# Kernel tuning notes

Hardware: AMD Instinct MI355X
Metric: run time of the kernel (lower is better)

Reference implementation:

```python
import jax, jax.numpy as jnp
import numpy as np

B, N, C = 2, 2048, 256
H_DIM, W_DIM = 64, 176


def _lin_init(k, fan_in, shape):
    return jax.random.normal(k, shape, dtype=jnp.float32) * (1.0 / np.sqrt(fan_in))


def setup_inputs() -> dict:
    key = jax.random.key(0)
    ks = jax.random.split(key, 12)
    # gaussian_data: (B, N, 14); positions [:3], sigma_x at 5, sigma_y at 6, weight at 12
    z = jax.random.uniform(ks[0], (B, N), minval=1.0, maxval=40.0)
    x = jax.random.uniform(ks[1], (B, N), minval=-0.6, maxval=0.6) * z
    y = jax.random.uniform(ks[2], (B, N), minval=-0.4, maxval=0.4) * z
    g = jax.random.normal(ks[3], (B, N, 14), dtype=jnp.float32)
    g = g.at[..., 0].set(x).at[..., 1].set(y).at[..., 2].set(z)
    g = g.at[..., 5].set(jax.random.uniform(ks[4], (B, N), minval=5.0, maxval=50.0))
    g = g.at[..., 6].set(jax.random.uniform(ks[5], (B, N), minval=5.0, maxval=50.0))
    g = g.at[..., 12].set(jax.random.uniform(ks[6], (B, N), minval=0.5, maxval=1.5))
    # pinhole intrinsic: fx=fy=1000, cx=880, cy=320
    intrinsic = jnp.array([[1000.0, 0.0, 880.0], [0.0, 1000.0, 320.0], [0.0, 0.0, 1.0]], dtype=jnp.float32)
    pk = jax.random.split(ks[7], 5)
    return {
        "gaussian_data": g,
        "intrinsic": intrinsic,
        "enc_w1": _lin_init(pk[0], 14, (14, 64)), "enc_b1": jnp.zeros((64,), jnp.float32),
        "enc_w2": _lin_init(pk[1], 64, (64, 128)), "enc_b2": jnp.zeros((128,), jnp.float32),
        "enc_w3": _lin_init(pk[2], 128, (128, C)), "enc_b3": jnp.zeros((C,), jnp.float32),
        "ft_w1": _lin_init(pk[3], C, (C, C)), "ft_b1": jnp.zeros((C,), jnp.float32),
        "ft_w2": _lin_init(pk[4], C, (C, C)), "ft_b2": jnp.zeros((C,), jnp.float32),
        "H": H_DIM, "W": W_DIM,
    }


def reference(gaussian_data, intrinsic, enc_w1, enc_b1, enc_w2, enc_b2, enc_w3, enc_b3,
              ft_w1, ft_b1, ft_w2, ft_b2, H, W):
    # Encoder MLP (dropout = identity in eval): (B,N,14) -> (B,N,C)
    h = jax.nn.relu(gaussian_data @ enc_w1 + enc_b1)
    h = jax.nn.relu(h @ enc_w2 + enc_b2)
    feats = h @ enc_w3 + enc_b3
    # feature_transform inside GaussianRadarProjection
    feats_t = jax.nn.relu(feats @ ft_w1 + ft_b1) @ ft_w2 + ft_b2  # (B,N,C)

    pos = gaussian_data[..., :3]                      # (B,N,3)
    valid = pos[..., 2] > 0.1                         # (B,N)
    proj = jnp.einsum('ij,bnj->bni', intrinsic, pos)  # (B,N,3)
    pts2d = proj[..., :2] / (proj[..., 2:3] + 1e-6)   # (B,N,2)
    scale_x = W / intrinsic[0, 2] / 2
    scale_y = H / intrinsic[1, 2] / 2
    px = pts2d[..., 0] * scale_x                      # (B,N)
    py = pts2d[..., 1] * scale_y
    inb = (px >= 0) & (px < W) & (py >= 0) & (py < H)
    mask = valid & inb                                # (B,N)

    sx = jnp.maximum(gaussian_data[..., 5] * scale_x, 1.0)  # (B,N)
    sy = jnp.maximum(gaussian_data[..., 6] * scale_y, 1.0)
    w = gaussian_data[..., 12]                               # (B,N)

    xg = jnp.arange(W, dtype=jnp.float32)
    yg = jnp.arange(H, dtype=jnp.float32)
    dx2 = ((xg[None, None, :] - px[..., None]) / sx[..., None]) ** 2  # (B,N,W)
    dy2 = ((yg[None, None, :] - py[..., None]) / sy[..., None]) ** 2  # (B,N,H)
    dist = dy2[..., :, None] + dx2[..., None, :]                      # (B,N,H,W)
    gw = jnp.exp(-0.5 * dist) * w[..., None, None]
    gw = gw * (dist < 9.0).astype(gw.dtype) * mask[..., None, None].astype(gw.dtype)

    density = jnp.sum(gw, axis=1)[:, None]                             # (B,1,H,W)
    feature_map = jnp.einsum('bnc,bnhw->bchw', feats_t, gw)            # (B,C,H,W)
    avg_sigma = (sx + sy) / 2                                          # (B,N)
    uncertainty = jnp.sum(gw * avg_sigma[..., None, None], axis=1)[:, None]

    density = jnp.clip(density, 1e-6)
    return feature_map / density, uncertainty / density, density
```

## Files before the change

### kernel.cpp

```cpp
#include <hip/hip_runtime.h>
#include <cstdint>
#include <cstddef>

#define B_ 2
#define N_ 2048
#define C_ 256
#define H_ 64
#define W_ 176
#define TW 16
#define NTX 11
#define NYB 32
#define NTILES2 (B_*NYB*NTX)
#define CAP 1024
#define SA 260
#define FS 40
#define CSTRIDE 16

typedef unsigned short ushort_t;
typedef short bf16x8 __attribute__((ext_vector_type(8)));
typedef float f32x4  __attribute__((ext_vector_type(4)));

__device__ __forceinline__ short f2bf(float f)
{
    unsigned u = __float_as_uint(f);
    return (short)((u + 0x7FFFu + ((u >> 16) & 1u)) >> 16);
}

__global__ __launch_bounds__(256)
void prep_kernel(const float* __restrict__ w3f, const float* __restrict__ fw1f,
                 const float* __restrict__ fw2f,
                 short* __restrict__ wt3, short* __restrict__ wt4,
                 short* __restrict__ wt5, int* __restrict__ counts)
{
    const int gid = blockIdx.x * 256 + threadIdx.x;
    if (gid < NTILES2 * CSTRIDE) counts[gid] = 0;
    for (int e = gid; e < 163840; e += 65536) {
        if (e < 32768) {
            const int k = e >> 8, n = e & 255;
            wt3[n * 128 + k] = f2bf(w3f[e]);
        } else if (e < 98304) {
            const int e2 = e - 32768;
            const int k = e2 >> 8, n = e2 & 255;
            wt4[n * 256 + k] = f2bf(fw1f[e2]);
        } else {
            const int e2 = e - 98304;
            const int k = e2 >> 8, n = e2 & 255;
            wt5[n * 256 + k] = f2bf(fw2f[e2]);
        }
    }
}

template<int K>
__device__ __forceinline__ void mfma_acc(const short* __restrict__ wt,
                                         const float* actIn, f32x4 (&acc)[2],
                                         int wv_, int quad, int ln15)
{
    bf16x8 wreg[K / 16];
#pragma unroll
    for (int ks = 0; ks < K / 32; ++ks) {
        const int kb = ks * 32 + quad * 8;
#pragma unroll
        for (int tt = 0; tt < 2; ++tt) {
            const int n0 = (wv_ * 2 + tt) * 16;
            wreg[ks * 2 + tt] = *(const bf16x8*)&wt[(size_t)(n0 + ln15) * K + kb];
        }
    }
#pragma unroll
    for (int ks = 0; ks < K / 32; ++ks) {
        const int kb = ks * 32 + quad * 8;
        const float4 a0 = *(const float4*)&actIn[ln15 * SA + kb];
        const float4 a1 = *(const float4*)&actIn[ln15 * SA + kb + 4];
        bf16x8 af = { f2bf(a0.x), f2bf(a0.y), f2bf(a0.z), f2bf(a0.w),
                      f2bf(a1.x), f2bf(a1.y), f2bf(a1.z), f2bf(a1.w) };
#pragma unroll
        for (int tt = 0; tt < 2; ++tt)
            acc[tt] = __builtin_amdgcn_mfma_f32_16x16x32_bf16(af, wreg[ks * 2 + tt],
                                                              acc[tt], 0, 0, 0);
    }
}

__global__ __launch_bounds__(512, 4)
void pb_mlp_kernel(const float* __restrict__ g, const float* __restrict__ intr,
                   const float* __restrict__ w1, const float* __restrict__ b1,
                   const float* __restrict__ w2, const float* __restrict__ b2,
                   const short* __restrict__ wt3, const float* __restrict__ b3,
                   const short* __restrict__ wt4, const float* __restrict__ fb1,
                   const short* __restrict__ wt5, const float* __restrict__ fb2,
                   ushort_t* __restrict__ ftb,
                   float* __restrict__ pp, int* __restrict__ counts,
                   ushort_t* __restrict__ lists)
{
    __shared__ __align__(16) float A_[16 * SA];
    __shared__ __align__(16) float Bb[16 * SA];
    const int tid = threadIdx.x;

    if (blockIdx.x < 256) {
        const int row0 = blockIdx.x * 16;
        const int lane = tid & 63;
        const int wv_  = tid >> 6;
        const int quad = lane >> 4;
        const int ln15 = lane & 15;

        if (tid < 224) {
            const int k = tid / 16, m = tid % 16;
            A_[m * SA + k] = g[(size_t)(row0 + m) * 14 + k];
        }
        __syncthreads();

        {
            const int col = tid & 63;
            const int m0  = (tid >> 6) * 2;
            float acc[2];
            const float bv = b1[col];
            acc[0] = bv; acc[1] = bv;
#pragma unroll
            for (int k = 0; k < 14; ++k) {
                const float wv = w1[k * 64 + col];
                acc[0] = fmaf(A_[(m0 + 0) * SA + k], wv, acc[0]);
                acc[1] = fmaf(A_[(m0 + 1) * SA + k], wv, acc[1]);
            }
            Bb[(m0 + 0) * SA + col] = fmaxf(acc[0], 0.f);
            Bb[(m0 + 1) * SA + col] = fmaxf(acc[1], 0.f);
        }
        __syncthreads();

        {
            const int col = tid & 127;
            const int m0  = (tid >> 7) * 4;
            float acc[4];
            const float bv = b2[col];
#pragma unroll
            for (int r = 0; r < 4; ++r) acc[r] = bv;
#pragma unroll 4
            for (int kq = 0; kq < 16; ++kq) {
                float wv[4];
#pragma unroll
                for (int jj = 0; jj < 4; ++jj) wv[jj] = w2[(4 * kq + jj) * 128 + col];
#pragma unroll
                for (int r = 0; r < 4; ++r) {
                    const float4 a4 = *(const float4*)&Bb[(m0 + r) * SA + 4 * kq];
                    acc[r] = fmaf(a4.x, wv[0], acc[r]);
                    acc[r] = fmaf(a4.y, wv[1], acc[r]);
                    acc[r] = fmaf(a4.z, wv[2], acc[r]);
                    acc[r] = fmaf(a4.w, wv[3], acc[r]);
                }
            }
#pragma unroll
            for (int r = 0; r < 4; ++r)
                A_[(m0 + r) * SA + col] = fmaxf(acc[r], 0.f);
        }
        __syncthreads();

        {
            f32x4 acc[2] = {{0,0,0,0},{0,0,0,0}};
            mfma_acc<128>(wt3, A_, acc, wv_, quad, ln15);
            __syncthreads();
#pragma unroll
            for (int tt = 0; tt < 2; ++tt) {
                const int n = (wv_ * 2 + tt) * 16 + ln15;
                const float bv = b3[n];
#pragma unroll
                for (int r = 0; r < 4; ++r)
                    Bb[(quad * 4 + r) * SA + n] = acc[tt][r] + bv;
            }
        }
        __syncthreads();

        {
            f32x4 acc[2] = {{0,0,0,0},{0,0,0,0}};
            mfma_acc<256>(wt4, Bb, acc, wv_, quad, ln15);
            __syncthreads();
#pragma unroll
            for (int tt = 0; tt < 2; ++tt) {
                const int n = (wv_ * 2 + tt) * 16 + ln15;
                const float bv = fb1[n];
#pragma unroll
                for (int r = 0; r < 4; ++r)
                    A_[(quad * 4 + r) * SA + n] = fmaxf(acc[tt][r] + bv, 0.f);
            }
        }
        __syncthreads();

        {
            f32x4 acc[2] = {{0,0,0,0},{0,0,0,0}};
            mfma_acc<256>(wt5, A_, acc, wv_, quad, ln15);
#pragma unroll
            for (int tt = 0; tt < 2; ++tt) {
                const int n = (wv_ * 2 + tt) * 16 + ln15;
                const float bv = fb2[n];
#pragma unroll
                for (int r = 0; r < 4; ++r)
                    ftb[(size_t)(row0 + quad * 4 + r) * 256 + n] =
                        (ushort_t)f2bf(acc[tt][r] + bv);
            }
        }
        return;
    }

    const int i = (blockIdx.x - 256) * 16 + (tid >> 5);
    const int j = tid & 31;
    const float* gi = g + (size_t)i * 14;
    const float x = gi[0], y = gi[1], z = gi[2];
    const float s5 = gi[5], s6 = gi[6], wv = gi[12];
    const float k00 = intr[0], k01 = intr[1], k02 = intr[2];
    const float k10 = intr[3], k11 = intr[4], k12 = intr[5];
    const float k20 = intr[6], k21 = intr[7], k22 = intr[8];
    const float projx = k00 * x + k01 * y + k02 * z;
    const float projy = k10 * x + k11 * y + k12 * z;
    const float projz = k20 * x + k21 * y + k22 * z;
    const float inv = 1.f / (projz + 1e-6f);
    const float scale_x = (float)W_ / k02 * 0.5f;
    const float scale_y = (float)H_ / k12 * 0.5f;
    const float px = projx * inv * scale_x;
    const float py = projy * inv * scale_y;
    const bool valid = z > 0.1f;
    const bool inb = (px >= 0.f) && (px < (float)W_) && (py >= 0.f) && (py < (float)H_);
    const bool mask = valid && inb;
    const float sx = fmaxf(s5 * scale_x, 1.f);
    const float sy = fmaxf(s6 * scale_y, 1.f);
    if (j == 0) {
        float4* o = (float4*)(pp + (size_t)i * 8);
        o[0] = make_float4(px, py, 1.f / sx, 1.f / sy);
        o[1] = make_float4(wv, 0.5f * (sx + sy), 0.f, 0.f);
    }
    if (!mask) return;
    const float rx = 3.f * sx, ry = 3.f * sy;
    const int ymin = max(0, (int)floorf(py - ry));
    const int ymax = min(H_ - 1, (int)ceilf(py + ry));
    const int bmin = ymin >> 1, bmax = ymax >> 1;
    const int band = bmin + j;
    if (band > bmax) return;
    const int tmin = max(0, (int)floorf((px - rx - (float)(TW - 1)) * (1.f / TW)));
    const int tmax = min(NTX - 1, (int)ceilf((px + rx) * (1.f / TW)));
    const int b = i / N_, n = i - b * N_;
    for (int t = tmin; t <= tmax; ++t) {
        const int tile = (b * NYB + band) * NTX + t;
        const int slot = atomicAdd(&counts[tile * CSTRIDE], 1);
        if (slot < CAP) lists[(size_t)tile * CAP + slot] = (ushort_t)n;
    }
}

__global__ __launch_bounds__(256)
void splat_kernel(const float* __restrict__ pp, const ushort_t* __restrict__ lists,
                  const int* __restrict__ counts, const ushort_t* __restrict__ ftb,
                  float* __restrict__ out)
{
    __shared__ __align__(16) ushort_t feats_t[2][256 * FS];
    __shared__ __align__(16) ushort_t gw_t[2][32 * FS];

    const int tid = threadIdx.x;
    const int qb = blockIdx.x;
    const int b  = qb & 1;
    const int t_ = qb >> 1;
    const int yr = t_ / NTX, xr = t_ % NTX;
    const int yh = (yr + 1) >> 1;
    const int yb = (yr & 1) ? (16 - yh) : (16 + yh);
    const int xh = (xr + 1) >> 1;
    const int txi = (xr & 1) ? (5 - xh) : (5 + xh);
    const int bid = (b * NYB + yb) * NTX + txi;
    const int y0 = yb * 2, x0 = txi * TW;

    const int cnt = min(counts[bid * CSTRIDE], CAP);
    const ushort_t* mylist = lists + (size_t)bid * CAP;
    const int gs   = tid >> 5;
    const int px32 = tid & 31;
    const float fy = (float)(y0 + (px32 >> 4));
    const float fx = (float)(x0 + (px32 & 15));
    const int chg = tid >> 4;
    const int qp  = tid & 15;
    const int bN = b * N_;
    const int lane = tid & 63;
    const int wv_  = tid >> 6;
    const int quad = lane >> 4;
    const int ln15 = lane & 15;

    f32x4 acc[2][4];
#pragma unroll
    for (int mt = 0; mt < 2; ++mt)
#pragma unroll
        for (int nt = 0; nt < 4; ++nt) acc[mt][nt] = (f32x4){0.f, 0.f, 0.f, 0.f};
    float densp = 0.f, uncp = 0.f;

    uint4 ra0, ra1, rb0, rb1;
    const int nchunks = (cnt + 31) >> 5;

    if (cnt > 0) {
        const float4* pv = (const float4*)pp;
        {
            const int n0 = mylist[min(2 * qp, cnt - 1)];
            const int n1 = mylist[min(2 * qp + 1, cnt - 1)];
            const uint4* f0 = (const uint4*)(ftb + ((size_t)(bN + n0) << 8) + chg * 16);
            const uint4* f1 = (const uint4*)(ftb + ((size_t)(bN + n1) << 8) + chg * 16);
            ra0 = f0[0]; ra1 = f0[1];
            rb0 = f1[0]; rb1 = f1[1];
        }
        for (int c = 0; c < nchunks; ++c) {
            const int buf = c & 1;
#pragma unroll
            for (int jj = 0; jj < 4; ++jj) {
                const int q = 8 * jj + gs;
                const int qi = c * 32 + q;
                const int n = mylist[min(qi, cnt - 1)];
                const float4 e0 = pv[(size_t)(bN + n) * 2 + 0];
                const float4 e1 = pv[(size_t)(bN + n) * 2 + 1];
                const float dyn = (fy - e0.y) * e0.w;
                const float dxn = (fx - e0.x) * e0.z;
                const float dist = dyn * dyn + dxn * dxn;
                float gv = 0.f;
                if (dist < 9.f) gv = __expf(-0.5f * dist) * e1.x;
                if (qi >= cnt) gv = 0.f;
                gw_t[buf][px32 * FS + q] = (ushort_t)f2bf(gv);
                densp += gv;
                uncp  += gv * e1.y;
            }
            {
                uint* dst = (uint*)&feats_t[buf][0];
#pragma unroll
                for (int jj = 0; jj < 4; ++jj) {
                    const uint u0 = (&ra0.x)[jj], v0 = (&rb0.x)[jj];
                    const int ch = chg * 16 + 2 * jj;
                    dst[ch * (FS / 2) + qp]       = (u0 & 0xffffu) | (v0 << 16);
                    dst[(ch + 1) * (FS / 2) + qp] = (u0 >> 16) | (v0 & 0xffff0000u);
                }
#pragma unroll
                for (int jj = 0; jj < 4; ++jj) {
                    const uint u0 = (&ra1.x)[jj], v0 = (&rb1.x)[jj];
                    const int ch = chg * 16 + 8 + 2 * jj;
                    dst[ch * (FS / 2) + qp]       = (u0 & 0xffffu) | (v0 << 16);
                    dst[(ch + 1) * (FS / 2) + qp] = (u0 >> 16) | (v0 & 0xffff0000u);
                }
            }
            __syncthreads();
            if (c + 1 < nchunks) {
                const int q0 = (c + 1) * 32 + 2 * qp;
                const int n0 = mylist[min(q0, cnt - 1)];
                const int n1 = mylist[min(q0 + 1, cnt - 1)];
                const uint4* f0 = (const uint4*)(ftb + ((size_t)(bN + n0) << 8) + chg * 16);
                const uint4* f1 = (const uint4*)(ftb + ((size_t)(bN + n1) << 8) + chg * 16);
                ra0 = f0[0]; ra1 = f0[1];
                rb0 = f1[0]; rb1 = f1[1];
            }
            bf16x8 af[2];
#pragma unroll
            for (int mt = 0; mt < 2; ++mt)
                af[mt] = *(const bf16x8*)&gw_t[buf][(mt * 16 + ln15) * FS + quad * 8];
#pragma unroll
            for (int nt = 0; nt < 4; ++nt) {
                const int ch0 = wv_ * 64 + nt * 16;
                const bf16x8 bf = *(const bf16x8*)&feats_t[buf][(ch0 + ln15) * FS + quad * 8];
                acc[0][nt] = __builtin_amdgcn_mfma_f32_16x16x32_bf16(af[0], bf, acc[0][nt], 0, 0, 0);
                acc[1][nt] = __builtin_amdgcn_mfma_f32_16x16x32_bf16(af[1], bf, acc[1][nt], 0, 0, 0);
            }
        }
    }

    __syncthreads();
    float* red_d = (float*)&feats_t[0][0];
    float* red_u = red_d + 8 * 36;
    red_d[gs * 36 + px32] = densp;
    red_u[gs * 36 + px32] = uncp;
    __syncthreads();
    for (int s = 4; s > 0; s >>= 1) {
        if (gs < s) {
            red_d[gs * 36 + px32] += red_d[(gs + s) * 36 + px32];
            red_u[gs * 36 + px32] += red_u[(gs + s) * 36 + px32];
        }
        __syncthreads();
    }

    if (tid < 32) {
        const int yy = y0 + (tid >> 4), xx = x0 + (tid & 15);
        const size_t pix = ((size_t)b * H_ + yy) * W_ + xx;
        float* unc_o = out + (size_t)B_ * C_ * H_ * W_;
        float* den_o = unc_o + (size_t)B_ * H_ * W_;
        const float d = fmaxf(red_d[tid], 1e-6f);
        unc_o[pix] = red_u[tid] / d;
        den_o[pix] = d;
    }

#pragma unroll
    for (int mt = 0; mt < 2; ++mt) {
        const int pxb = mt * 16 + quad * 4;
        float rinv[4];
#pragma unroll
        for (int r = 0; r < 4; ++r)
            rinv[r] = 1.f / fmaxf(red_d[pxb + r], 1e-6f);
        const int yy = y0 + mt;
#pragma unroll
        for (int nt = 0; nt < 4; ++nt) {
            const int ch = wv_ * 64 + nt * 16 + ln15;
            float4 v;
            v.x = acc[mt][nt][0] * rinv[0];
            v.y = acc[mt][nt][1] * rinv[1];
            v.z = acc[mt][nt][2] * rinv[2];
            v.w = acc[mt][nt][3] * rinv[3];
            *(float4*)(out + (((size_t)b * C_ + ch) * H_ + yy) * W_
                       + x0 + quad * 4) = v;
        }
    }
}

extern "C" void kernel_launch(void* const* d_in, const int* in_sizes, int n_in,
                              void* d_out, int out_size, void* d_ws, size_t ws_size,
                              hipStream_t stream)
{
    const float* g    = (const float*)d_in[0];
    const float* intr = (const float*)d_in[1];
    const float* w1   = (const float*)d_in[2];
    const float* b1   = (const float*)d_in[3];
    const float* w2   = (const float*)d_in[4];
    const float* b2   = (const float*)d_in[5];
    const float* w3   = (const float*)d_in[6];
    const float* b3   = (const float*)d_in[7];
    const float* fw1  = (const float*)d_in[8];
    const float* fb1  = (const float*)d_in[9];
    const float* fw2  = (const float*)d_in[10];
    const float* fb2  = (const float*)d_in[11];

    char* base = (char*)d_ws;
    const int rows = B_ * N_;
    ushort_t* ftb = (ushort_t*)base;
    float* pp     = (float*)(base + (size_t)rows * C_ * 2);
    int*   counts = (int*)(pp + (size_t)8 * rows);
    ushort_t* lists = (ushort_t*)(counts + NTILES2 * CSTRIDE);
    short* wt3    = (short*)(lists + (size_t)NTILES2 * CAP);
    short* wt4    = wt3 + 128 * 256;
    short* wt5    = wt4 + 256 * 256;

    prep_kernel<<<dim3(256), dim3(256), 0, stream>>>(w3, fw1, fw2, wt3, wt4, wt5, counts);
    pb_mlp_kernel<<<dim3(512), dim3(512), 0, stream>>>(
        g, intr, w1, b1, w2, b2, wt3, b3, wt4, fb1, wt5, fb2, ftb, pp, counts, lists);
    splat_kernel<<<dim3(NTILES2), dim3(256), 0, stream>>>(pp, lists, counts, ftb, (float*)d_out);
}
```

Baseline: 139.7 us.

## Split per-tile binning counters into sub-buckets to reduce atomic contention

```diff
diff --git a/kernel.cpp b/kernel.cpp
--- a/kernel.cpp
+++ b/kernel.cpp
@@ -11,7 +11,8 @@
 #define NTX 11
 #define NYB 32
 #define NTILES2 (B_*NYB*NTX)
-#define CAP 1024
+#define NSUB 8
+#define SUBCAP 256
 #define SA 260
 #define FS 40
 #define CSTRIDE 16
@@ -33,7 +34,7 @@
                  short* __restrict__ wt5, int* __restrict__ counts)
 {
     const int gid = blockIdx.x * 256 + threadIdx.x;
-    if (gid < NTILES2 * CSTRIDE) counts[gid] = 0;
+    for (int c = gid; c < NTILES2 * NSUB * CSTRIDE; c += 65536) counts[c] = 0;
     for (int e = gid; e < 163840; e += 65536) {
         if (e < 32768) {
             const int k = e >> 8, n = e & 255;
@@ -197,6 +198,7 @@
         return;
     }
 
+    const int sub = (blockIdx.x - 256) & (NSUB - 1);
     const int i = (blockIdx.x - 256) * 16 + (tid >> 5);
     const int j = tid & 31;
     const float* gi = g + (size_t)i * 14;
@@ -235,8 +237,9 @@
     const int b = i / N_, n = i - b * N_;
     for (int t = tmin; t <= tmax; ++t) {
         const int tile = (b * NYB + band) * NTX + t;
-        const int slot = atomicAdd(&counts[tile * CSTRIDE], 1);
-        if (slot < CAP) lists[(size_t)tile * CAP + slot] = (ushort_t)n;
+        const int slot = atomicAdd(&counts[(tile * NSUB + sub) * CSTRIDE], 1);
+        if (slot < SUBCAP)
+            lists[((size_t)tile * NSUB + sub) * SUBCAP + slot] = (ushort_t)n;
     }
 }
 
@@ -247,6 +250,7 @@
 {
     __shared__ __align__(16) ushort_t feats_t[2][256 * FS];
     __shared__ __align__(16) ushort_t gw_t[2][32 * FS];
+    __shared__ __align__(16) ushort_t list_s[NSUB * SUBCAP];
 
     const int tid = threadIdx.x;
     const int qb = blockIdx.x;
@@ -257,11 +261,21 @@
     const int yb = (yr & 1) ? (16 - yh) : (16 + yh);
     const int xh = (xr + 1) >> 1;
     const int txi = (xr & 1) ? (5 - xh) : (5 + xh);
-    const int bid = (b * NYB + yb) * NTX + txi;
+    const int tb  = (b * NYB + yb) * NTX + txi;
     const int y0 = yb * 2, x0 = txi * TW;
 
-    const int cnt = min(counts[bid * CSTRIDE], CAP);
-    const ushort_t* mylist = lists + (size_t)bid * CAP;
+    int tot = 0;
+#pragma unroll
+    for (int s = 0; s < NSUB; ++s) {
+        const int cs = min(counts[(tb * NSUB + s) * CSTRIDE], SUBCAP);
+        const ushort_t* src = lists + ((size_t)tb * NSUB + s) * SUBCAP;
+        for (int k = tid; k < cs; k += 256) list_s[tot + k] = src[k];
+        tot += cs;
+    }
+    __syncthreads();
+    const int cnt = tot;
+
+    const ushort_t* mylist = list_s;
     const int gs   = tid >> 5;
     const int px32 = tid & 31;
     const float fy = (float)(y0 + (px32 >> 4));
@@ -422,8 +436,8 @@
     ushort_t* ftb = (ushort_t*)base;
     float* pp     = (float*)(base + (size_t)rows * C_ * 2);
     int*   counts = (int*)(pp + (size_t)8 * rows);
-    ushort_t* lists = (ushort_t*)(counts + NTILES2 * CSTRIDE);
-    short* wt3    = (short*)(lists + (size_t)NTILES2 * CAP);
+    ushort_t* lists = (ushort_t*)(counts + NTILES2 * NSUB * CSTRIDE);
+    short* wt3    = (short*)(lists + (size_t)NTILES2 * NSUB * SUBCAP);
     short* wt4    = wt3 + 128 * 256;
     short* wt5    = wt4 + 256 * 256;
 
```

Measured after the change: 133.9 us. -4.2%, faster.
